# Performance work log

Hardware: AMD Instinct MI355X
Metric: run time of the kernel (lower is better)

The kernel has to match this reference:

```python
import jax, jax.numpy as jnp
import numpy as np

T = 1_000_000  # sequence length
H = 5          # LSTM hidden size
NC = 4         # number of channel streams (all fed through lstm1, as in the original)


def setup_inputs() -> dict:
    key = jax.random.key(0)
    ks = jax.random.split(key, 14)
    s = 1.0 / np.sqrt(H)  # PyTorch default LSTM/Linear init scale
    u = lambda k, shape: jax.random.uniform(k, shape, jnp.float32, -s, s)
    sf1 = 1.0 / np.sqrt(20.0)
    sf2 = 1.0 / np.sqrt(10.0)
    return {
        "inputs": jax.random.normal(ks[0], (T, 1, NC), jnp.float32),
        # lstm1 layer 0: input_size=1
        "w_ih0": u(ks[1], (4 * H, 1)),
        "w_hh0": u(ks[2], (4 * H, H)),
        "b_ih0": u(ks[3], (4 * H,)),
        "b_hh0": u(ks[4], (4 * H,)),
        # lstm1 layer 1: input_size=H
        "w_ih1": u(ks[5], (4 * H, H)),
        "w_hh1": u(ks[6], (4 * H, H)),
        "b_ih1": u(ks[7], (4 * H,)),
        "b_hh1": u(ks[8], (4 * H,)),
        "fc1_w": jax.random.uniform(ks[9], (10, 20), jnp.float32, -sf1, sf1),
        "fc1_b": jax.random.uniform(ks[10], (10,), jnp.float32, -sf1, sf1),
        "fc2_w": jax.random.uniform(ks[11], (1, 10), jnp.float32, -sf2, sf2),
        "fc2_b": jax.random.uniform(ks[12], (1,), jnp.float32, -sf2, sf2),
    }


def _lstm_layer(x_seq, w_ih, w_hh, b_ih, b_hh):
    """Single PyTorch-style LSTM layer. x_seq: (T, B, in) -> h_seq: (T, B, H)."""
    # Input projection for all timesteps at once (outside the scan).
    gx = jnp.einsum('tbi,gi->tbg', x_seq, w_ih) + b_ih + b_hh  # (T, B, 4H)

    def step(carry, gx_t):
        h, c = carry
        g = gx_t + h @ w_hh.T                      # (B, 4H)
        i, f, gg, o = jnp.split(g, 4, axis=-1)     # PyTorch gate order i,f,g,o
        i = jax.nn.sigmoid(i)
        f = jax.nn.sigmoid(f)
        gg = jnp.tanh(gg)
        o = jax.nn.sigmoid(o)
        c = f * c + i * gg
        h = o * jnp.tanh(c)
        return (h, c), h

    B = x_seq.shape[1]
    z = jnp.zeros((B, H), x_seq.dtype)
    _, h_seq = jax.lax.scan(step, (z, z), gx)
    return h_seq


def reference(inputs, w_ih0, w_hh0, b_ih0, b_hh0, w_ih1, w_hh1, b_ih1, b_hh1,
              fc1_w, fc1_b, fc2_w, fc2_b):
    # Original code runs all 4 channel streams through lstm1 (lstm2-4 unused),
    # so we fold the 4 streams into the LSTM batch dim: (T, 4, 1).
    x = inputs[:, 0, :, None]                      # (T, NC, 1)
    h = _lstm_layer(x, w_ih0, w_hh0, b_ih0, b_hh0)  # (T, NC, H)
    h = _lstm_layer(h, w_ih1, w_hh1, b_ih1, b_hh1)  # (T, NC, H)
    # torch.cat((out1..out4), dim=2) on (T,1,H) slices == channel-major reshape
    out_cat = h.reshape(T, 1, NC * H)              # (T, 1, 20)
    out = out_cat @ fc1_w.T + fc1_b                # (T, 1, 10)
    out = out @ fc2_w.T + fc2_b                    # (T, 1, 1)
    return out
```

## Files before the change

### kernel.cpp

```cpp
#include <hip/hip_runtime.h>

#define T_TOTAL 1000000
#define NCHUNK  6144
#define CLEN    163
#define WARM    24


typedef float v2 __attribute__((ext_vector_type(2)));

#define L2E  1.44269504088896340736f
#define K2   2.88539008177792681472f

__device__ __forceinline__ float bperm(int addr4, float v) {
    return __int_as_float(__builtin_amdgcn_ds_bpermute(addr4, __float_as_int(v)));
}
__device__ __forceinline__ v2 pkfma(v2 a, v2 b, v2 c) {
    return __builtin_elementwise_fma(a, b, c);
}

__global__ __launch_bounds__(64, 1) void lstm_chunks(
    const float* __restrict__ inp,
    const float* __restrict__ wih0,
    const float* __restrict__ whh0,
    const float* __restrict__ bih0,
    const float* __restrict__ bhh0,
    const float* __restrict__ wih1,
    const float* __restrict__ whh1,
    const float* __restrict__ bih1,
    const float* __restrict__ bhh1,
    const float* __restrict__ fc1w,
    const float* __restrict__ fc1b,
    const float* __restrict__ fc2w,
    const float* __restrict__ fc2b,
    float* __restrict__ out)
{
    const int lane = threadIdx.x & 63;
    int cw = lane / 20; if (cw > 2) cw = 2;
    int q  = lane - cw * 20; if (q > 19) q = 19;
    const int b = q / 5;
    const int j = q % 5;
    const int chunk = blockIdx.x * 3 + cw;
    const int base  = cw * 20;

    int gh[5];
    #pragma unroll
    for (int k = 0; k < 5; ++k) gh[k] = (base + b * 5 + k) * 4;
    const int rd5  = (lane + 5)  * 4;
    const int rd10 = (lane + 10) * 4;

    v2 W0x01, W0x23, BB001, BB023, BB101, BB123;
    v2 W0h01[5], W0h23[5], W1a01[5], W1a23[5], W1b01[5], W1b23[5];
    {
        const int r0 = j, r1 = 5 + j, r2 = 10 + j, r3 = 15 + j;
        const v2 s01 = v2{-L2E, -L2E};
        const v2 s23 = v2{-K2,  -L2E};
        W0x01 = s01 * v2{wih0[r0], wih0[r1]};
        W0x23 = s23 * v2{wih0[r2], wih0[r3]};
        BB001 = s01 * v2{bih0[r0] + bhh0[r0], bih0[r1] + bhh0[r1]};
        BB023 = s23 * v2{bih0[r2] + bhh0[r2], bih0[r3] + bhh0[r3]};
        BB101 = s01 * v2{bih1[r0] + bhh1[r0], bih1[r1] + bhh1[r1]};
        BB123 = s23 * v2{bih1[r2] + bhh1[r2], bih1[r3] + bhh1[r3]};
        #pragma unroll
        for (int k = 0; k < 5; ++k) {
            W0h01[k] = s01 * v2{whh0[r0 * 5 + k], whh0[r1 * 5 + k]};
            W0h23[k] = s23 * v2{whh0[r2 * 5 + k], whh0[r3 * 5 + k]};
            W1a01[k] = s01 * v2{wih1[r0 * 5 + k], wih1[r1 * 5 + k]};
            W1a23[k] = s23 * v2{wih1[r2 * 5 + k], wih1[r3 * 5 + k]};
            W1b01[k] = s01 * v2{whh1[r0 * 5 + k], whh1[r1 * 5 + k]};
            W1b23[k] = s23 * v2{whh1[r2 * 5 + k], whh1[r3 * 5 + k]};
        }
    }
    float vb[5] = {0, 0, 0, 0, 0};
    float sc = fc2b[0];
    #pragma unroll
    for (int m = 0; m < 10; ++m) {
        const float f2 = fc2w[m];
        sc = __builtin_fmaf(f2, fc1b[m], sc);
        #pragma unroll
        for (int k = 0; k < 5; ++k)
            vb[k] = __builtin_fmaf(f2, fc1w[m * 20 + b * 5 + k], vb[k]);
    }

    const int o_begin = chunk * CLEN;
    const int warm = (chunk == 0) ? 0 : WARM;

    float C0 = 0.0f, C1 = 0.0f;
    float h0r[5] = {0, 0, 0, 0, 0};
    float h1A[5] = {0, 0, 0, 0, 0};
    float h1B[5] = {0, 0, 0, 0, 0};

    auto ldx = [&](int t_) -> float {
        const int tt = (t_ > T_TOTAL - 1) ? (T_TOTAL - 1) : t_;
        return inp[(size_t)tt * 4 + b];
    };

    auto cellp = [&](v2 A01, v2 A23, float& C) -> float {
        const float ei = __builtin_amdgcn_exp2f(A01.x);
        const float ef = __builtin_amdgcn_exp2f(A01.y);
        const float eg = __builtin_amdgcn_exp2f(A23.x);
        const float eo = __builtin_amdgcn_exp2f(A23.y);
        const float Di = 1.0f + ei, Df = 1.0f + ef, Dg = 1.0f + eg, Do = 1.0f + eo;
        const float p1 = Di * Df, p2 = Dg * Do, p3 = Df * Do;
        const float r  = __builtin_amdgcn_rcpf(p1 * p2);
        const float f  = (Di * p2) * r;
        const float o  = (p1 * Dg) * r;
        const float tg = __builtin_fmaf(K2, eg, -K2);
        C = __builtin_fmaf(f, C, (tg * p3) * r);
        const float eh = __builtin_amdgcn_exp2f(C);
        return (o * (1.0f - eh)) * __builtin_amdgcn_rcpf(1.0f + eh);
    };

    auto matvec0 = [&](float x, const float (&h)[5], v2& A01, v2& A23) {
        const v2 xx = v2{x, x};
        v2 P01 = pkfma(W0x01, xx, BB001);
        v2 P23 = pkfma(W0x23, xx, BB023);
        const v2 k0 = v2{h[0], h[0]}, k1 = v2{h[1], h[1]};
        const v2 k2 = v2{h[2], h[2]}, k3 = v2{h[3], h[3]};
        const v2 k4 = v2{h[4], h[4]};
        P01 = pkfma(W0h01[0], k0, P01);  v2 Q01 = W0h01[2] * k2;
        P23 = pkfma(W0h23[0], k0, P23);  v2 Q23 = W0h23[2] * k2;
        P01 = pkfma(W0h01[1], k1, P01);  Q01 = pkfma(W0h01[3], k3, Q01);
        P23 = pkfma(W0h23[1], k1, P23);  Q23 = pkfma(W0h23[3], k3, Q23);
        Q01 = pkfma(W0h01[4], k4, Q01);
        Q23 = pkfma(W0h23[4], k4, Q23);
        A01 = P01 + Q01; A23 = P23 + Q23;
    };
    auto matvec1 = [&](const float (&h0)[5], const float (&h1)[5], v2& A01, v2& A23) {
        v2 P01 = BB101, P23 = BB123;
        const v2 g0 = v2{h1[0], h1[0]};
        v2 Q01 = W1b01[0] * g0;
        v2 Q23 = W1b23[0] * g0;
        #pragma unroll
        for (int k = 0; k < 5; ++k) {
            const v2 hk = v2{h0[k], h0[k]};
            P01 = pkfma(W1a01[k], hk, P01);
            P23 = pkfma(W1a23[k], hk, P23);
        }
        #pragma unroll
        for (int k = 1; k < 5; ++k) {
            const v2 gk = v2{h1[k], h1[k]};
            Q01 = pkfma(W1b01[k], gk, Q01);
            Q23 = pkfma(W1b23[k], gk, Q23);
        }
        A01 = P01 + Q01; A23 = P23 + Q23;
    };

    int t = o_begin - warm;
    {
        v2 A01, A23;
        matvec0(ldx(t), h0r, A01, A23);
        const float h0 = cellp(A01, A23, C0);
        #pragma unroll
        for (int k = 0; k < 5; ++k) h0r[k] = bperm(gh[k], h0);
    }
    float xc = ldx(t + 1);

    #define STEP(H1IN, H1OUT, EMIT)                                            \
    {                                                                          \
        v2 A01, A23;                                                           \
        matvec1(h0r, H1IN, A01, A23);                                          \
        const float h1 = cellp(A01, A23, C1);                                  \
        _Pragma("unroll")                                                      \
        for (int k = 0; k < 5; ++k) H1OUT[k] = bperm(gh[k], h1);               \
        const float xn = ldx(t + 2);                                           \
        matvec0(xc, h0r, A01, A23);                                            \
        const float h0 = cellp(A01, A23, C0);                                  \
        _Pragma("unroll")                                                      \
        for (int k = 0; k < 5; ++k) h0r[k] = bperm(gh[k], h0);                 \
        xc = xn;                                                               \
        if (EMIT) {                                                            \
            float p = vb[0] * H1OUT[0];                                        \
            p = __builtin_fmaf(vb[1], H1OUT[1], p);                            \
            p = __builtin_fmaf(vb[2], H1OUT[2], p);                            \
            p = __builtin_fmaf(vb[3], H1OUT[3], p);                            \
            p = __builtin_fmaf(vb[4], H1OUT[4], p);                            \
            const float u = p + bperm(rd5, p);                                 \
            const float S = u + bperm(rd10, u);                                \
            if (q == 0 && t < T_TOTAL) out[t] = S + sc;                        \
        }                                                                      \
        ++t;                                                                   \
    }

    for (int i = 0; i < warm; i += 2) { STEP(h1A, h1B, false) STEP(h1B, h1A, false) }
    for (int i = 0; i < CLEN - 1; i += 2) { STEP(h1A, h1B, true) STEP(h1B, h1A, true) }
    STEP(h1A, h1B, true)

    #undef STEP
}

extern "C" void kernel_launch(void* const* d_in, const int* in_sizes, int n_in,
                              void* d_out, int out_size, void* d_ws, size_t ws_size,
                              hipStream_t stream) {
    (void)in_sizes; (void)n_in; (void)d_ws; (void)ws_size; (void)out_size;
    lstm_chunks<<<NCHUNK / 3, 64, 0, stream>>>(
        (const float*)d_in[0],  (const float*)d_in[1],  (const float*)d_in[2],
        (const float*)d_in[3],  (const float*)d_in[4],  (const float*)d_in[5],
        (const float*)d_in[6],  (const float*)d_in[7],  (const float*)d_in[8],
        (const float*)d_in[9],  (const float*)d_in[10], (const float*)d_in[11],
        (const float*)d_in[12], (float*)d_out);
}
```

Before: 185.9 us.

## Interleave two independent sequence chunks per wave for instruction-level parallelism

Each wavefront now advances two chunks, one from each half of the sequence, in lockstep inside one unrolled step, and the grid is halved. The intent is to fill the latency gaps of the serial LSTM recurrence (exp/rcp, packed FMAs, ds_bpermute) with independent work from the second chunk, instead of relying on a second wave per SIMD. Chunk 0 now runs the warm-up too and then resets its state, so all lanes follow uniform control flow. The cost is roughly double the register use per wave and fewer waves in flight, so latency hiding across waves is lost.

After: 202.4 us. 1.09x slower.

```diff
diff --git a/kernel.cpp b/kernel.cpp
--- a/kernel.cpp
+++ b/kernel.cpp
@@ -39,8 +39,9 @@
     int q  = lane - cw * 20; if (q > 19) q = 19;
     const int b = q / 5;
     const int j = q % 5;
-    const int chunk = blockIdx.x * 3 + cw;
-    const int base  = cw * 20;
+    const int chunkA = blockIdx.x * 3 + cw;
+    const int chunkB = chunkA + (NCHUNK / 2);
+    const int base   = cw * 20;
 
     int gh[5];
     #pragma unroll
@@ -81,15 +82,19 @@
             vb[k] = __builtin_fmaf(f2, fc1w[m * 20 + b * 5 + k], vb[k]);
     }
 
-    const int o_begin = chunk * CLEN;
-    const int warm = (chunk == 0) ? 0 : WARM;
-
-    float C0 = 0.0f, C1 = 0.0f;
-    float h0r[5] = {0, 0, 0, 0, 0};
-    float h1A[5] = {0, 0, 0, 0, 0};
-    float h1B[5] = {0, 0, 0, 0, 0};
-
-    auto ldx = [&](int t_) -> float {
+    float C0a = 0.0f, C1a = 0.0f, C0b = 0.0f, C1b = 0.0f;
+    float h0ra[5] = {0, 0, 0, 0, 0}, h0rb[5] = {0, 0, 0, 0, 0};
+    float h1Aa[5] = {0, 0, 0, 0, 0}, h1Ba[5] = {0, 0, 0, 0, 0};
+    float h1Ab[5] = {0, 0, 0, 0, 0}, h1Bb[5] = {0, 0, 0, 0, 0};
+
+    int ta = chunkA * CLEN - WARM;
+    int tb = chunkB * CLEN - WARM;
+
+    auto ldxA = [&](int t_) -> float {
+        const int tt = (t_ < 0) ? 0 : t_;
+        return inp[(size_t)tt * 4 + b];
+    };
+    auto ldxB = [&](int t_) -> float {
         const int tt = (t_ > T_TOTAL - 1) ? (T_TOTAL - 1) : t_;
         return inp[(size_t)tt * 4 + b];
     };
@@ -145,54 +150,96 @@
         A01 = P01 + Q01; A23 = P23 + Q23;
     };
 
-    int t = o_begin - warm;
+    float xca, xcb;
     {
+        v2 Aa01, Aa23, Ab01, Ab23;
+        matvec0(ldxA(ta), h0ra, Aa01, Aa23);
+        matvec0(ldxB(tb), h0rb, Ab01, Ab23);
+        const float h0a = cellp(Aa01, Aa23, C0a);
+        const float h0b = cellp(Ab01, Ab23, C0b);
+        #pragma unroll
+        for (int k = 0; k < 5; ++k) h0ra[k] = bperm(gh[k], h0a);
+        #pragma unroll
+        for (int k = 0; k < 5; ++k) h0rb[k] = bperm(gh[k], h0b);
+        xca = ldxA(ta + 1);
+        xcb = ldxB(tb + 1);
+    }
+
+    #define STEP2(IA, OA, IB, OB, EMIT)                                        \
+    {                                                                          \
+        v2 Aa01, Aa23, Ab01, Ab23;                                             \
+        matvec1(h0ra, IA, Aa01, Aa23);                                         \
+        matvec1(h0rb, IB, Ab01, Ab23);                                         \
+        const float h1a = cellp(Aa01, Aa23, C1a);                              \
+        const float h1b = cellp(Ab01, Ab23, C1b);                              \
+        _Pragma("unroll")                                                      \
+        for (int k = 0; k < 5; ++k) OA[k] = bperm(gh[k], h1a);                 \
+        _Pragma("unroll")                                                      \
+        for (int k = 0; k < 5; ++k) OB[k] = bperm(gh[k], h1b);                 \
+        const float xna = ldxA(ta + 2);                                        \
+        const float xnb = ldxB(tb + 2);                                        \
+        matvec0(xca, h0ra, Aa01, Aa23);                                        \
+        matvec0(xcb, h0rb, Ab01, Ab23);                                        \
+        const float h0a = cellp(Aa01, Aa23, C0a);                              \
+        const float h0b = cellp(Ab01, Ab23, C0b);                              \
+        _Pragma("unroll")                                                      \
+        for (int k = 0; k < 5; ++k) h0ra[k] = bperm(gh[k], h0a);               \
+        _Pragma("unroll")                                                      \
+        for (int k = 0; k < 5; ++k) h0rb[k] = bperm(gh[k], h0b);               \
+        xca = xna; xcb = xnb;                                                  \
+        if (EMIT) {                                                            \
+            float pa = vb[0] * OA[0];                                          \
+            pa = __builtin_fmaf(vb[1], OA[1], pa);                             \
+            pa = __builtin_fmaf(vb[2], OA[2], pa);                             \
+            pa = __builtin_fmaf(vb[3], OA[3], pa);                             \
+            pa = __builtin_fmaf(vb[4], OA[4], pa);                             \
+            float pb = vb[0] * OB[0];                                          \
+            pb = __builtin_fmaf(vb[1], OB[1], pb);                             \
+            pb = __builtin_fmaf(vb[2], OB[2], pb);                             \
+            pb = __builtin_fmaf(vb[3], OB[3], pb);                             \
+            pb = __builtin_fmaf(vb[4], OB[4], pb);                             \
+            const float ua = pa + bperm(rd5, pa);                              \
+            const float ub = pb + bperm(rd5, pb);                              \
+            const float Sa = ua + bperm(rd10, ua);                             \
+            const float Sb = ub + bperm(rd10, ub);                             \
+            if (q == 0) out[ta] = Sa + sc;                  \
+            if (q == 0 && tb < T_TOTAL) out[tb] = Sb + sc;                     \
+        }                                                                      \
+        ++ta; ++tb;                                                            \
+    }
+
+    for (int i = 0; i < WARM; i += 2) {
+        STEP2(h1Aa, h1Ba, h1Ab, h1Bb, false)
+        STEP2(h1Ba, h1Aa, h1Bb, h1Ab, false)
+    }
+
+    if (chunkA == 0) {
+        C0a = 0.0f; C1a = 0.0f;
+        #pragma unroll
+        for (int k = 0; k < 5; ++k) { h1Aa[k] = 0.0f; h1Ba[k] = 0.0f; }
+        float z[5] = {0, 0, 0, 0, 0};
         v2 A01, A23;
-        matvec0(ldx(t), h0r, A01, A23);
-        const float h0 = cellp(A01, A23, C0);
-        #pragma unroll
-        for (int k = 0; k < 5; ++k) h0r[k] = bperm(gh[k], h0);
-    }
-    float xc = ldx(t + 1);
-
-    #define STEP(H1IN, H1OUT, EMIT)                                            \
-    {                                                                          \
-        v2 A01, A23;                                                           \
-        matvec1(h0r, H1IN, A01, A23);                                          \
-        const float h1 = cellp(A01, A23, C1);                                  \
-        _Pragma("unroll")                                                      \
-        for (int k = 0; k < 5; ++k) H1OUT[k] = bperm(gh[k], h1);               \
-        const float xn = ldx(t + 2);                                           \
-        matvec0(xc, h0r, A01, A23);                                            \
-        const float h0 = cellp(A01, A23, C0);                                  \
-        _Pragma("unroll")                                                      \
-        for (int k = 0; k < 5; ++k) h0r[k] = bperm(gh[k], h0);                 \
-        xc = xn;                                                               \
-        if (EMIT) {                                                            \
-            float p = vb[0] * H1OUT[0];                                        \
-            p = __builtin_fmaf(vb[1], H1OUT[1], p);                            \
-            p = __builtin_fmaf(vb[2], H1OUT[2], p);                            \
-            p = __builtin_fmaf(vb[3], H1OUT[3], p);                            \
-            p = __builtin_fmaf(vb[4], H1OUT[4], p);                            \
-            const float u = p + bperm(rd5, p);                                 \
-            const float S = u + bperm(rd10, u);                                \
-            if (q == 0 && t < T_TOTAL) out[t] = S + sc;                        \
-        }                                                                      \
-        ++t;                                                                   \
-    }
-
-    for (int i = 0; i < warm; i += 2) { STEP(h1A, h1B, false) STEP(h1B, h1A, false) }
-    for (int i = 0; i < CLEN - 1; i += 2) { STEP(h1A, h1B, true) STEP(h1B, h1A, true) }
-    STEP(h1A, h1B, true)
-
-    #undef STEP
+        matvec0(inp[b], z, A01, A23);
+        const float h0 = cellp(A01, A23, C0a);
+        #pragma unroll
+        for (int k = 0; k < 5; ++k) h0ra[k] = bperm(gh[k], h0);
+        xca = inp[4 + b];
+    }
+
+    for (int i = 0; i < CLEN - 1; i += 2) {
+        STEP2(h1Aa, h1Ba, h1Ab, h1Bb, true)
+        STEP2(h1Ba, h1Aa, h1Bb, h1Ab, true)
+    }
+    STEP2(h1Aa, h1Ba, h1Ab, h1Bb, true)
+
+    #undef STEP2
 }
 
 extern "C" void kernel_launch(void* const* d_in, const int* in_sizes, int n_in,
                               void* d_out, int out_size, void* d_ws, size_t ws_size,
                               hipStream_t stream) {
     (void)in_sizes; (void)n_in; (void)d_ws; (void)ws_size; (void)out_size;
-    lstm_chunks<<<NCHUNK / 3, 64, 0, stream>>>(
+    lstm_chunks<<<NCHUNK / 6, 64, 0, stream>>>(
         (const float*)d_in[0],  (const float*)d_in[1],  (const float*)d_in[2],
         (const float*)d_in[3],  (const float*)d_in[4],  (const float*)d_in[5],
         (const float*)d_in[6],  (const float*)d_in[7],  (const float*)d_in[8],
```

## Exchange hidden states through LDS and double the number of chunks

Applied to the files above, without the earlier changes.

Hidden-state broadcast moves from five ds_bpermute calls per layer per step to one LDS write plus vector LDS reads. Chunk count doubles while chunk length halves, giving more wavefronts and a shorter serial chain per chunk. The warmup overhead per output grows, and the first chunk now resets its state after warmup. The emitted output is delayed by one step to line up with the new read order. Correctness relies on lockstep execution within a single wave, since there is no barrier between the LDS write and the next read.

Result: slower. 195.9 us (+5.4%).

```diff
diff --git a/kernel.cpp b/kernel.cpp
--- a/kernel.cpp
+++ b/kernel.cpp
@@ -1,12 +1,13 @@
 #include <hip/hip_runtime.h>
 
 #define T_TOTAL 1000000
-#define NCHUNK  6144
-#define CLEN    163
+#define NCHUNK  12288
+#define CLEN    82
 #define WARM    24
 
 
 typedef float v2 __attribute__((ext_vector_type(2)));
+typedef float v4 __attribute__((ext_vector_type(4)));
 
 #define L2E  1.44269504088896340736f
 #define K2   2.88539008177792681472f
@@ -34,17 +35,18 @@
     const float* __restrict__ fc2b,
     float* __restrict__ out)
 {
+    __shared__ float hsh[408];
+
     const int lane = threadIdx.x & 63;
     int cw = lane / 20; if (cw > 2) cw = 2;
     int q  = lane - cw * 20; if (q > 19) q = 19;
     const int b = q / 5;
     const int j = q % 5;
     const int chunk = blockIdx.x * 3 + cw;
-    const int base  = cw * 20;
-
-    int gh[5];
-    #pragma unroll
-    for (int k = 0; k < 5; ++k) gh[k] = (base + b * 5 + k) * 4;
+
+    const int rw = cw * 68 + b * 8;
+    const int ww = rw + j;
+
     const int rd5  = (lane + 5)  * 4;
     const int rd10 = (lane + 10) * 4;
 
@@ -81,16 +83,12 @@
             vb[k] = __builtin_fmaf(f2, fc1w[m * 20 + b * 5 + k], vb[k]);
     }
 
-    const int o_begin = chunk * CLEN;
-    const int warm = (chunk == 0) ? 0 : WARM;
-
     float C0 = 0.0f, C1 = 0.0f;
-    float h0r[5] = {0, 0, 0, 0, 0};
-    float h1A[5] = {0, 0, 0, 0, 0};
-    float h1B[5] = {0, 0, 0, 0, 0};
+    int t = chunk * CLEN - WARM;
 
     auto ldx = [&](int t_) -> float {
-        const int tt = (t_ > T_TOTAL - 1) ? (T_TOTAL - 1) : t_;
+        int tt = t_ < 0 ? 0 : t_;
+        tt = tt > T_TOTAL - 1 ? T_TOTAL - 1 : tt;
         return inp[(size_t)tt * 4 + b];
     };
 
@@ -145,45 +143,65 @@
         A01 = P01 + Q01; A23 = P23 + Q23;
     };
 
-    int t = o_begin - warm;
+    hsh[ww + 204] = 0.0f;
     {
+        float z[5] = {0, 0, 0, 0, 0};
         v2 A01, A23;
-        matvec0(ldx(t), h0r, A01, A23);
-        const float h0 = cellp(A01, A23, C0);
-        #pragma unroll
-        for (int k = 0; k < 5; ++k) h0r[k] = bperm(gh[k], h0);
+        matvec0(ldx(t), z, A01, A23);
+        const float h0n = cellp(A01, A23, C0);
+        hsh[ww] = h0n;
     }
     float xc = ldx(t + 1);
 
-    #define STEP(H1IN, H1OUT, EMIT)                                            \
+    #define STEP(EMIT)                                                         \
     {                                                                          \
+        float h0v[5], h1v[5];                                                  \
+        {                                                                      \
+            const v4 a0 = *(const v4*)&hsh[rw];                                \
+            const v4 a1 = *(const v4*)&hsh[rw + 204];                          \
+            h0v[0] = a0[0]; h0v[1] = a0[1]; h0v[2] = a0[2]; h0v[3] = a0[3];    \
+            h0v[4] = hsh[rw + 4];                                              \
+            h1v[0] = a1[0]; h1v[1] = a1[1]; h1v[2] = a1[2]; h1v[3] = a1[3];    \
+            h1v[4] = hsh[rw + 204 + 4];                                        \
+        }                                                                      \
         v2 A01, A23;                                                           \
-        matvec1(h0r, H1IN, A01, A23);                                          \
-        const float h1 = cellp(A01, A23, C1);                                  \
-        _Pragma("unroll")                                                      \
-        for (int k = 0; k < 5; ++k) H1OUT[k] = bperm(gh[k], h1);               \
+        matvec1(h0v, h1v, A01, A23);                                           \
+        const float h1n = cellp(A01, A23, C1);                                 \
+        hsh[ww + 204] = h1n;                                                   \
         const float xn = ldx(t + 2);                                           \
-        matvec0(xc, h0r, A01, A23);                                            \
-        const float h0 = cellp(A01, A23, C0);                                  \
-        _Pragma("unroll")                                                      \
-        for (int k = 0; k < 5; ++k) h0r[k] = bperm(gh[k], h0);                 \
+        matvec0(xc, h0v, A01, A23);                                            \
+        const float h0n = cellp(A01, A23, C0);                                 \
+        hsh[ww] = h0n;                                                         \
         xc = xn;                                                               \
         if (EMIT) {                                                            \
-            float p = vb[0] * H1OUT[0];                                        \
-            p = __builtin_fmaf(vb[1], H1OUT[1], p);                            \
-            p = __builtin_fmaf(vb[2], H1OUT[2], p);                            \
-            p = __builtin_fmaf(vb[3], H1OUT[3], p);                            \
-            p = __builtin_fmaf(vb[4], H1OUT[4], p);                            \
+            float p = vb[0] * h1v[0];                                          \
+            p = __builtin_fmaf(vb[1], h1v[1], p);                              \
+            p = __builtin_fmaf(vb[2], h1v[2], p);                              \
+            p = __builtin_fmaf(vb[3], h1v[3], p);                              \
+            p = __builtin_fmaf(vb[4], h1v[4], p);                              \
             const float u = p + bperm(rd5, p);                                 \
             const float S = u + bperm(rd10, u);                                \
-            if (q == 0 && t < T_TOTAL) out[t] = S + sc;                        \
+            if (q == 0 && (t - 1) < T_TOTAL) out[t - 1] = S + sc;              \
         }                                                                      \
         ++t;                                                                   \
     }
 
-    for (int i = 0; i < warm; i += 2) { STEP(h1A, h1B, false) STEP(h1B, h1A, false) }
-    for (int i = 0; i < CLEN - 1; i += 2) { STEP(h1A, h1B, true) STEP(h1B, h1A, true) }
-    STEP(h1A, h1B, true)
+    for (int i = 0; i < WARM; ++i) STEP(false)
+
+    if (blockIdx.x == 0 && cw == 0) {
+        C0 = 0.0f; C1 = 0.0f;
+        hsh[ww + 204] = 0.0f;
+        float z[5] = {0, 0, 0, 0, 0};
+        v2 A01, A23;
+        matvec0(inp[b], z, A01, A23);
+        const float h0n = cellp(A01, A23, C0);
+        hsh[ww] = h0n;
+        xc = inp[4 + b];
+    }
+
+    STEP(false)
+
+    for (int i = 0; i < CLEN; ++i) STEP(true)
 
     #undef STEP
 }
```

## Fuse both layers' cell math with shared reciprocals and use more, shorter chunks

Applied to the files above, without the earlier changes.

Each step now evaluates the layer-0 and layer-1 gate activations together and shares one reciprocal across both layers' gate denominators and another across both tanh denominators. This halves the number of rcp instructions per step and exposes more independent work to hide transcendental latency. The chunk count also rises and chunk length shrinks so more wavefronts run in parallel, at the cost of a larger share of warm-up steps. Multiplying more denominators together before the reciprocal raises the risk of overflow or precision loss.

Measured after the change: 192.7 us. 1.04x slower.

```diff
diff --git a/kernel.cpp b/kernel.cpp
--- a/kernel.cpp
+++ b/kernel.cpp
@@ -1,8 +1,8 @@
 #include <hip/hip_runtime.h>
 
 #define T_TOTAL 1000000
-#define NCHUNK  6144
-#define CLEN    163
+#define NCHUNK  9216
+#define CLEN    109
 #define WARM    24
 
 
@@ -17,6 +17,8 @@
 __device__ __forceinline__ v2 pkfma(v2 a, v2 b, v2 c) {
     return __builtin_elementwise_fma(a, b, c);
 }
+__device__ __forceinline__ float ex2(float x) { return __builtin_amdgcn_exp2f(x); }
+__device__ __forceinline__ float rcp(float x) { return __builtin_amdgcn_rcpf(x); }
 
 __global__ __launch_bounds__(64, 1) void lstm_chunks(
     const float* __restrict__ inp,
@@ -94,22 +96,6 @@
         return inp[(size_t)tt * 4 + b];
     };
 
-    auto cellp = [&](v2 A01, v2 A23, float& C) -> float {
-        const float ei = __builtin_amdgcn_exp2f(A01.x);
-        const float ef = __builtin_amdgcn_exp2f(A01.y);
-        const float eg = __builtin_amdgcn_exp2f(A23.x);
-        const float eo = __builtin_amdgcn_exp2f(A23.y);
-        const float Di = 1.0f + ei, Df = 1.0f + ef, Dg = 1.0f + eg, Do = 1.0f + eo;
-        const float p1 = Di * Df, p2 = Dg * Do, p3 = Df * Do;
-        const float r  = __builtin_amdgcn_rcpf(p1 * p2);
-        const float f  = (Di * p2) * r;
-        const float o  = (p1 * Dg) * r;
-        const float tg = __builtin_fmaf(K2, eg, -K2);
-        C = __builtin_fmaf(f, C, (tg * p3) * r);
-        const float eh = __builtin_amdgcn_exp2f(C);
-        return (o * (1.0f - eh)) * __builtin_amdgcn_rcpf(1.0f + eh);
-    };
-
     auto matvec0 = [&](float x, const float (&h)[5], v2& A01, v2& A23) {
         const v2 xx = v2{x, x};
         v2 P01 = pkfma(W0x01, xx, BB001);
@@ -145,6 +131,20 @@
         A01 = P01 + Q01; A23 = P23 + Q23;
     };
 
+    auto cellp = [&](v2 A01, v2 A23, float& C) -> float {
+        const float ei = ex2(A01.x), ef = ex2(A01.y);
+        const float eg = ex2(A23.x), eo = ex2(A23.y);
+        const float Di = 1.0f + ei, Df = 1.0f + ef, Dg = 1.0f + eg, Do = 1.0f + eo;
+        const float p1 = Di * Df, p2 = Dg * Do, p3 = Df * Do;
+        const float r  = rcp(p1 * p2);
+        const float f  = (Di * p2) * r;
+        const float o  = (p1 * Dg) * r;
+        const float tg = __builtin_fmaf(K2, eg, -K2);
+        C = __builtin_fmaf(f, C, (tg * p3) * r);
+        const float eh = ex2(C);
+        return (o * (1.0f - eh)) * rcp(1.0f + eh);
+    };
+
     int t = o_begin - warm;
     {
         v2 A01, A23;
@@ -157,14 +157,36 @@
 
     #define STEP(H1IN, H1OUT, EMIT)                                            \
     {                                                                          \
-        v2 A01, A23;                                                           \
-        matvec1(h0r, H1IN, A01, A23);                                          \
-        const float h1 = cellp(A01, A23, C1);                                  \
+        v2 A101, A123, A001, A023;                                             \
+        matvec1(h0r, H1IN, A101, A123);                                        \
+        matvec0(xc, h0r, A001, A023);                                          \
+        const float xn = ldx(t + 2);                                           \
+        const float e1i = ex2(A101.x), e1f = ex2(A101.y);                      \
+        const float e1g = ex2(A123.x), e1o = ex2(A123.y);                      \
+        const float e0i = ex2(A001.x), e0f = ex2(A001.y);                      \
+        const float e0g = ex2(A023.x), e0o = ex2(A023.y);                      \
+        const float D1i = 1.0f + e1i, D1f = 1.0f + e1f;                        \
+        const float D1g = 1.0f + e1g, D1o = 1.0f + e1o;                        \
+        const float D0i = 1.0f + e0i, D0f = 1.0f + e0f;                        \
+        const float D0g = 1.0f + e0g, D0o = 1.0f + e0o;                        \
+        const float p11 = D1i * D1f, p12 = D1g * D1o, p13 = D1f * D1o;         \
+        const float p01 = D0i * D0f, p02 = D0g * D0o, p03 = D0f * D0o;         \
+        const float P1 = p11 * p12, P0 = p01 * p02;                            \
+        const float r8 = rcp(P1 * P0);                                         \
+        const float r1 = r8 * P0, r0 = r8 * P1;                                \
+        const float f1 = (D1i * p12) * r1, o1 = (p11 * D1g) * r1;              \
+        const float tg1 = __builtin_fmaf(K2, e1g, -K2);                        \
+        C1 = __builtin_fmaf(f1, C1, (tg1 * p13) * r1);                         \
+        const float f0 = (D0i * p02) * r0, o0 = (p01 * D0g) * r0;              \
+        const float tg0 = __builtin_fmaf(K2, e0g, -K2);                        \
+        C0 = __builtin_fmaf(f0, C0, (tg0 * p03) * r0);                         \
+        const float eh1 = ex2(C1), eh0 = ex2(C0);                              \
+        const float E1 = 1.0f + eh1, E0 = 1.0f + eh0;                          \
+        const float rr = rcp(E1 * E0);                                         \
+        const float h1 = (o1 * (1.0f - eh1)) * (E0 * rr);                      \
+        const float h0 = (o0 * (1.0f - eh0)) * (E1 * rr);                      \
         _Pragma("unroll")                                                      \
         for (int k = 0; k < 5; ++k) H1OUT[k] = bperm(gh[k], h1);               \
-        const float xn = ldx(t + 2);                                           \
-        matvec0(xc, h0r, A01, A23);                                            \
-        const float h0 = cellp(A01, A23, C0);                                  \
         _Pragma("unroll")                                                      \
         for (int k = 0; k < 5; ++k) h0r[k] = bperm(gh[k], h0);                 \
         xc = xn;                                                               \
```
